# Performance work log

Hardware: AMD Instinct MI355X
Metric: run time of the kernel (lower is better)

Reference implementation:

```python
import jax, jax.numpy as jnp
import numpy as np

N_NODES = 100000


def gcn_conv(x, edge_index, W, b):
    """PyG-style GCNConv: linear transform, add self-loops, symmetric deg
    normalization, scatter-add aggregation, bias."""
    N = x.shape[0]
    h = x @ W  # [N, out]
    loops = jnp.arange(N, dtype=edge_index.dtype)
    src = jnp.concatenate([edge_index[0], loops])  # message sources (x_j)
    dst = jnp.concatenate([edge_index[1], loops])  # aggregation targets
    ones = jnp.ones(src.shape[0], dtype=h.dtype)
    deg = jax.ops.segment_sum(ones, dst, num_segments=N)
    dinv = jnp.where(deg > 0, jax.lax.rsqrt(deg), 0.0)
    norm = dinv[src] * dinv[dst]  # [E+N]
    msgs = h[src] * norm[:, None]  # gather + scale
    out = jax.ops.segment_sum(msgs, dst, num_segments=N)  # scatter-add
    return out + b


def setup_inputs() -> dict:
    key = jax.random.key(0)
    k1, k2, k3, k4, k5 = jax.random.split(key, 5)
    N, E, D, H = N_NODES, 3200000, 16, 16
    x = jax.random.normal(k1, (N, D), dtype=jnp.float32)
    edge_index = jax.random.randint(k2, (2, E), 0, N, dtype=jnp.int64)
    W1 = jax.random.normal(k3, (D, H), dtype=jnp.float32) / np.sqrt(D)
    b1 = jnp.zeros((H,), dtype=jnp.float32)
    W2 = jax.random.normal(k4, (H, 1), dtype=jnp.float32) / np.sqrt(H)
    b2 = jnp.zeros((1,), dtype=jnp.float32)
    return {"x": x, "edge_index": edge_index, "W1": W1, "b1": b1, "W2": W2, "b2": b2}


def reference(x, edge_index, W1, b1, W2, b2):
    h = jax.nn.relu(gcn_conv(x, edge_index, W1, b1))
    out = gcn_conv(h, edge_index, W2, b2)
    return jnp.squeeze(out, axis=-1)  # [N]
```

## Files before the change

kernel.cpp:

```cpp
#include <hip/hip_runtime.h>
#include <hip/hip_fp16.h>
#include <stdint.h>

#define TPB 256
#define TPBP 512
#define TPBR 512
#define NPB 256
#define LOG_NPB 8
#define MAXBINS 400
#define NCHUNK 512
#define CHUNK_CAP 6400
#define PCAP 48
#define PB2CAP 9216
#define START_MASK 0x1FFFFFFu

__global__ __launch_bounds__(TPBP) void k_place(const int* __restrict__ ei, int E,
                                                int chunkE, int nbins,
                                                int* __restrict__ baseT,
                                                uint32_t* __restrict__ part) {
    __shared__ uint32_t stage[CHUNK_CAP];
    __shared__ int sstart[MAXBINS];
    __shared__ int scnt[MAXBINS];
    __shared__ int scur[MAXBINS];
    int c = blockIdx.x, t = threadIdx.x;
    int es = c * chunkE, ee = min(E, es + chunkE), n = ee - es;
    for (int i = t; i < nbins; i += TPBP) scur[i] = 0;
    __syncthreads();
    const int* srcs = ei + es;
    const int* dsts = ei + E + es;
    int nv = n >> 2;
    bool al = ((((uintptr_t)srcs) | ((uintptr_t)dsts)) & 15) == 0;
    int4 sb[4], db[4];
    if (al) {
        const int4* s4 = (const int4*)srcs;
        const int4* d4 = (const int4*)dsts;
#pragma unroll
        for (int j = 0; j < 4; ++j) {
            int i = t + j * TPBP;
            if (i < nv) { sb[j] = s4[i]; db[j] = d4[i]; }
        }
#pragma unroll
        for (int j = 0; j < 4; ++j) {
            int i = t + j * TPBP;
            if (i < nv) {
                atomicAdd(&scur[db[j].x >> LOG_NPB], 1);
                atomicAdd(&scur[db[j].y >> LOG_NPB], 1);
                atomicAdd(&scur[db[j].z >> LOG_NPB], 1);
                atomicAdd(&scur[db[j].w >> LOG_NPB], 1);
            }
        }
        for (int i = 4 * nv + t; i < n; i += TPBP)
            atomicAdd(&scur[dsts[i] >> LOG_NPB], 1);
    } else {
        for (int i = t; i < n; i += TPBP)
            atomicAdd(&scur[dsts[i] >> LOG_NPB], 1);
    }
    __syncthreads();
    int val = (t < nbins) ? scur[t] : 0;
    __syncthreads();
    for (int off = 1; off < TPBP; off <<= 1) {
        int add = 0;
        if (t < nbins && t >= off) add = scur[t - off];
        __syncthreads();
        if (t < nbins) scur[t] += add;
        __syncthreads();
    }
    if (t < nbins) {
        sstart[t] = scur[t] - val;
        scnt[t] = val;
        baseT[(size_t)c * nbins + t] = val;
    }
    __syncthreads();
    if (t < nbins) scur[t] = sstart[t];
    __syncthreads();
    if (al) {
#pragma unroll
        for (int j = 0; j < 4; ++j) {
            int i = t + j * TPBP;
            if (i < nv) {
                int slot;
                slot = atomicAdd(&scur[db[j].x >> LOG_NPB], 1);
                stage[slot] = ((uint32_t)sb[j].x << LOG_NPB) | (uint32_t)(db[j].x & (NPB - 1));
                slot = atomicAdd(&scur[db[j].y >> LOG_NPB], 1);
                stage[slot] = ((uint32_t)sb[j].y << LOG_NPB) | (uint32_t)(db[j].y & (NPB - 1));
                slot = atomicAdd(&scur[db[j].z >> LOG_NPB], 1);
                stage[slot] = ((uint32_t)sb[j].z << LOG_NPB) | (uint32_t)(db[j].z & (NPB - 1));
                slot = atomicAdd(&scur[db[j].w >> LOG_NPB], 1);
                stage[slot] = ((uint32_t)sb[j].w << LOG_NPB) | (uint32_t)(db[j].w & (NPB - 1));
            }
        }
        for (int i = 4 * nv + t; i < n; i += TPBP) {
            int s = srcs[i], d = dsts[i];
            int slot = atomicAdd(&scur[d >> LOG_NPB], 1);
            stage[slot] = ((uint32_t)s << LOG_NPB) | (uint32_t)(d & (NPB - 1));
        }
    } else {
        for (int i = t; i < n; i += TPBP) {
            int s = srcs[i], d = dsts[i];
            int slot = atomicAdd(&scur[d >> LOG_NPB], 1);
            stage[slot] = ((uint32_t)s << LOG_NPB) | (uint32_t)(d & (NPB - 1));
        }
    }
    __syncthreads();
    int q = t >> 4, l = t & 15;
    for (int b = q; b < nbins; b += (TPBP >> 4)) {
        int l0 = sstart[b];
        int len = min(scnt[b], PCAP);
        size_t g0 = (size_t)b * ((size_t)NCHUNK * PCAP) + (size_t)c * PCAP;
        for (int i = l; i < len; i += 16)
            part[g0 + i] = stage[l0 + i];
    }
}

__global__ __launch_bounds__(TPBR) void k_rows(const uint32_t* __restrict__ part,
                                               const int* __restrict__ baseT,
                                               const float* __restrict__ x,
                                               const float* __restrict__ W1,
                                               uint32_t* __restrict__ rowInfo,
                                               float* __restrict__ dinv,
                                               int* __restrict__ part2,
                                               __half* __restrict__ g1h,
                                               int N, int nbins) {
    __shared__ int cnt[NPB];
    __shared__ int sbuf[NPB];
    __shared__ int cur[NPB];
    __shared__ int stage2[PB2CAP];
    __shared__ float Ws[256];
    int b = blockIdx.x, t = threadIdx.x;
    if (t < 256) Ws[t] = W1[t];
    if (t < NPB) cnt[t] = 0;
    __syncthreads();
    int my = min(baseT[(size_t)t * nbins + b], PCAP);
    const uint32_t* seg = part + (size_t)b * ((size_t)NCHUNK * PCAP) + (size_t)t * PCAP;
    for (int i = 0; i < my; ++i)
        atomicAdd(&cnt[seg[i] & (NPB - 1)], 1);
    __syncthreads();
    int deg = (t < NPB) ? cnt[t] : 0;
    if (t < NPB) sbuf[t] = deg;
    __syncthreads();
    for (int off = 1; off < NPB; off <<= 1) {
        int add = 0;
        if (t < NPB && t >= off) add = sbuf[t - off];
        __syncthreads();
        if (t < NPB) sbuf[t] += add;
        __syncthreads();
    }
    int excl = 0, total;
    if (t < NPB) {
        excl = sbuf[t] - deg;
        cur[t] = excl;
    }
    total = min(sbuf[NPB - 1], PB2CAP);
    int node = b * NPB + (t & (NPB - 1));
    float dv = rsqrtf(1.0f + (float)deg);
    if (t < NPB && node < N) {
        uint32_t dg = (uint32_t)min(deg, 127);
        rowInfo[node] = ((uint32_t)(b * PB2CAP + excl) & START_MASK) | (dg << 25);
        dinv[node] = dv;
    }
    __syncthreads();
    for (int i = 0; i < my; ++i) {
        uint32_t v = seg[i];
        int slot = atomicAdd(&cur[v & (NPB - 1)], 1);
        if (slot < PB2CAP) stage2[slot] = (int)(v >> LOG_NPB);
    }
    __syncthreads();
    int* p2 = part2 + (size_t)b * PB2CAP;
    for (int i = t; i < total; i += TPBR) p2[i] = stage2[i];
    if (t < NPB && node < N) {
        const float4* xv = (const float4*)(x + (size_t)node * 16);
        float4 a = xv[0], bb = xv[1], cc = xv[2], dd = xv[3];
        float xi[16] = {a.x, a.y, a.z, a.w, bb.x, bb.y, bb.z, bb.w,
                        cc.x, cc.y, cc.z, cc.w, dd.x, dd.y, dd.z, dd.w};
        __half2 hp[8];
#pragma unroll
        for (int j = 0; j < 8; ++j) {
            float o0 = 0.f, o1 = 0.f;
#pragma unroll
            for (int k = 0; k < 16; ++k) {
                o0 += xi[k] * Ws[k * 16 + 2 * j];
                o1 += xi[k] * Ws[k * 16 + 2 * j + 1];
            }
            hp[j] = __floats2half2_rn(o0 * dv, o1 * dv);
        }
        uint4* dst = (uint4*)(g1h + (size_t)node * 16);
        dst[0] = *(uint4*)&hp[0];
        dst[1] = *(uint4*)&hp[4];
    }
}

__global__ __launch_bounds__(256) void k_agg1_csr(const int* __restrict__ part2,
                                                  const uint32_t* __restrict__ rowInfo,
                                                  const __half* __restrict__ g1h,
                                                  const float* __restrict__ dinv,
                                                  const float* __restrict__ b1,
                                                  const float* __restrict__ W2,
                                                  float* __restrict__ g2, int N) {
    int wave = threadIdx.x >> 6, lane = threadIdx.x & 63;
    int n = blockIdx.x * 4 + wave;
    if (n >= N) return;
    int sub = lane >> 2;
    int j   = lane & 3;
    uint32_t info = rowInfo[n];
    int e0 = (int)(info & START_MASK);
    int e1 = e0 + (int)(info >> 25);
    float a0 = 0.f, a1 = 0.f, a2 = 0.f, a3 = 0.f;
    int e = e0 + sub;
    for (; e + 16 < e1; e += 32) {
        int s0 = part2[e];
        int s1 = part2[e + 16];
        uint2 u0 = *(const uint2*)(g1h + (size_t)s0 * 16 + 4 * j);
        uint2 u1 = *(const uint2*)(g1h + (size_t)s1 * 16 + 4 * j);
        float2 f;
        f = __half22float2(*(__half2*)&u0.x); a0 += f.x; a1 += f.y;
        f = __half22float2(*(__half2*)&u0.y); a2 += f.x; a3 += f.y;
        f = __half22float2(*(__half2*)&u1.x); a0 += f.x; a1 += f.y;
        f = __half22float2(*(__half2*)&u1.y); a2 += f.x; a3 += f.y;
    }
    for (; e < e1; e += 16) {
        int s0 = part2[e];
        uint2 u0 = *(const uint2*)(g1h + (size_t)s0 * 16 + 4 * j);
        float2 f;
        f = __half22float2(*(__half2*)&u0.x); a0 += f.x; a1 += f.y;
        f = __half22float2(*(__half2*)&u0.y); a2 += f.x; a3 += f.y;
    }
#pragma unroll
    for (int m = 4; m < 64; m <<= 1) {
        a0 += __shfl_xor(a0, m);
        a1 += __shfl_xor(a1, m);
        a2 += __shfl_xor(a2, m);
        a3 += __shfl_xor(a3, m);
    }
    {
        uint2 us = *(const uint2*)(g1h + (size_t)n * 16 + 4 * j);
        float2 f;
        f = __half22float2(*(__half2*)&us.x); a0 += f.x; a1 += f.y;
        f = __half22float2(*(__half2*)&us.y); a2 += f.x; a3 += f.y;
    }
    float di = dinv[n];
    float4 b1v = ((const float4*)b1)[j];
    float4 w2v = ((const float4*)W2)[j];
    float p = fmaxf(fmaf(a0, di, b1v.x), 0.f) * w2v.x
            + fmaxf(fmaf(a1, di, b1v.y), 0.f) * w2v.y
            + fmaxf(fmaf(a2, di, b1v.z), 0.f) * w2v.z
            + fmaxf(fmaf(a3, di, b1v.w), 0.f) * w2v.w;
    p += __shfl_xor(p, 1);
    p += __shfl_xor(p, 2);
    if (lane == 0) g2[n] = p * di;
}

__global__ __launch_bounds__(256) void k_agg2_csr(const int* __restrict__ part2,
                                                  const uint32_t* __restrict__ rowInfo,
                                                  const float* __restrict__ g2,
                                                  const float* __restrict__ dinv,
                                                  const float* __restrict__ b2,
                                                  float* __restrict__ out, int N) {
    int q = threadIdx.x >> 4, l = threadIdx.x & 15;
    int n = blockIdx.x * 16 + q;
    if (n >= N) return;
    uint32_t info = rowInfo[n];
    int e0 = (int)(info & START_MASK);
    int e1 = e0 + (int)(info >> 25);
    float acc = 0.f;
    for (int e = e0 + l; e < e1; e += 16)
        acc += g2[part2[e]];
    acc += __shfl_xor(acc, 1);
    acc += __shfl_xor(acc, 2);
    acc += __shfl_xor(acc, 4);
    acc += __shfl_xor(acc, 8);
    if (l == 0) out[n] = (acc + g2[n]) * dinv[n] + b2[0];
}

extern "C" void kernel_launch(void* const* d_in, const int* in_sizes, int n_in,
                              void* d_out, int out_size, void* d_ws, size_t ws_size,
                              hipStream_t stream) {
    const float* x  = (const float*)d_in[0];
    const int*   ei = (const int*)d_in[1];
    const float* W1 = (const float*)d_in[2];
    const float* b1 = (const float*)d_in[3];
    const float* W2 = (const float*)d_in[4];
    const float* b2 = (const float*)d_in[5];
    float* out = (float*)d_out;

    const int N = in_sizes[0] / 16;
    const int E = in_sizes[1] / 2;
    const int nbins = (N + NPB - 1) / NPB;
    const int chunkE = (((E + NCHUNK - 1) / NCHUNK) + 15) & ~15;

    float*    dinv    = (float*)d_ws;
    __half*   g1h     = (__half*)(dinv + N);
    uint32_t* part    = (uint32_t*)(g1h + (size_t)16 * N);
    int*      part2   = (int*)(part + (size_t)nbins * NCHUNK * PCAP);
    int*      baseT   = part2 + (size_t)nbins * PB2CAP;
    uint32_t* rowInfo = (uint32_t*)(baseT + (size_t)NCHUNK * nbins);
    float*    g2      = (float*)(rowInfo + N);

    k_place<<<NCHUNK, TPBP, 0, stream>>>(ei, E, chunkE, nbins, baseT, part);
    k_rows<<<nbins, TPBR, 0, stream>>>(part, baseT, x, W1, rowInfo, dinv, part2, g1h, N, nbins);
    k_agg1_csr<<<(N + 3) / 4, TPB, 0, stream>>>(part2, rowInfo, g1h, dinv, b1, W2, g2, N);
    k_agg2_csr<<<(N + 15) / 16, TPB, 0, stream>>>(part2, rowInfo, g2, dinv, b2, out, N);
}
```

Measured before the change: 170.1 us.

## Stage partition bins cooperatively in LDS and widen agg1 gathers to 16-byte loads

```diff
diff --git a/kernel.cpp b/kernel.cpp
--- a/kernel.cpp
+++ b/kernel.cpp
@@ -121,19 +121,47 @@
                                                int* __restrict__ part2,
                                                __half* __restrict__ g1h,
                                                int N, int nbins) {
+    __shared__ uint32_t stage2[PB2CAP];
+    __shared__ int scnt[NCHUNK];
+    __shared__ int soff[NCHUNK];
     __shared__ int cnt[NPB];
     __shared__ int sbuf[NPB];
     __shared__ int cur[NPB];
-    __shared__ int stage2[PB2CAP];
     __shared__ float Ws[256];
     int b = blockIdx.x, t = threadIdx.x;
     if (t < 256) Ws[t] = W1[t];
     if (t < NPB) cnt[t] = 0;
-    __syncthreads();
     int my = min(baseT[(size_t)t * nbins + b], PCAP);
-    const uint32_t* seg = part + (size_t)b * ((size_t)NCHUNK * PCAP) + (size_t)t * PCAP;
-    for (int i = 0; i < my; ++i)
-        atomicAdd(&cnt[seg[i] & (NPB - 1)], 1);
+    scnt[t] = my;
+    soff[t] = my;
+    __syncthreads();
+    for (int off = 1; off < TPBR; off <<= 1) {
+        int add = (t >= off) ? soff[t - off] : 0;
+        __syncthreads();
+        soff[t] += add;
+        __syncthreads();
+    }
+    int total = min(soff[TPBR - 1], PB2CAP);
+    int excl_s = soff[t] - my;
+    __syncthreads();
+    soff[t] = excl_s;
+    __syncthreads();
+    {
+        int g = t >> 4, l = t & 15;
+        const uint32_t* binBase = part + (size_t)b * ((size_t)NCHUNK * PCAP);
+        for (int s = g; s < NCHUNK; s += (TPBR >> 4)) {
+            int c2 = scnt[s];
+            int bs = soff[s];
+            const uint32_t* seg = binBase + (size_t)s * PCAP;
+            for (int i = l; i < c2; i += 16) {
+                int o = bs + i;
+                if (o < PB2CAP) stage2[o] = seg[i];
+            }
+        }
+    }
+    __syncthreads();
+    for (int i = t; i < total; i += TPBR)
+        atomicAdd(&cnt[stage2[i] & (NPB - 1)], 1);
     __syncthreads();
     int deg = (t < NPB) ? cnt[t] : 0;
     if (t < NPB) sbuf[t] = deg;
@@ -145,28 +173,24 @@
         if (t < NPB) sbuf[t] += add;
         __syncthreads();
     }
-    int excl = 0, total;
-    if (t < NPB) {
-        excl = sbuf[t] - deg;
-        cur[t] = excl;
-    }
-    total = min(sbuf[NPB - 1], PB2CAP);
     int node = b * NPB + (t & (NPB - 1));
     float dv = rsqrtf(1.0f + (float)deg);
-    if (t < NPB && node < N) {
-        uint32_t dg = (uint32_t)min(deg, 127);
-        rowInfo[node] = ((uint32_t)(b * PB2CAP + excl) & START_MASK) | (dg << 25);
-        dinv[node] = dv;
-    }
-    __syncthreads();
-    for (int i = 0; i < my; ++i) {
-        uint32_t v = seg[i];
+    if (t < NPB) {
+        int excl = sbuf[t] - deg;
+        cur[t] = excl;
+        if (node < N) {
+            uint32_t dg = (uint32_t)min(deg, 127);
+            rowInfo[node] = ((uint32_t)(b * PB2CAP + excl) & START_MASK) | (dg << 25);
+            dinv[node] = dv;
+        }
+    }
+    __syncthreads();
+    int* p2 = part2 + (size_t)b * PB2CAP;
+    for (int i = t; i < total; i += TPBR) {
+        uint32_t v = stage2[i];
         int slot = atomicAdd(&cur[v & (NPB - 1)], 1);
-        if (slot < PB2CAP) stage2[slot] = (int)(v >> LOG_NPB);
-    }
-    __syncthreads();
-    int* p2 = part2 + (size_t)b * PB2CAP;
-    for (int i = t; i < total; i += TPBR) p2[i] = stage2[i];
+        p2[slot] = (int)(v >> LOG_NPB);
+    }
     if (t < NPB && node < N) {
         const float4* xv = (const float4*)(x + (size_t)node * 16);
         float4 a = xv[0], bb = xv[1], cc = xv[2], dd = xv[3];
@@ -199,53 +223,57 @@
     int wave = threadIdx.x >> 6, lane = threadIdx.x & 63;
     int n = blockIdx.x * 4 + wave;
     if (n >= N) return;
-    int sub = lane >> 2;
-    int j   = lane & 3;
+    int j = lane & 1;
+    int sub = lane >> 1;
     uint32_t info = rowInfo[n];
     int e0 = (int)(info & START_MASK);
     int e1 = e0 + (int)(info >> 25);
     float a0 = 0.f, a1 = 0.f, a2 = 0.f, a3 = 0.f;
+    float a4 = 0.f, a5 = 0.f, a6 = 0.f, a7 = 0.f;
     int e = e0 + sub;
-    for (; e + 16 < e1; e += 32) {
+#define ACC8(U) { float2 f;                                            \
+        f = __half22float2(*(__half2*)&(U).x); a0 += f.x; a1 += f.y;   \
+        f = __half22float2(*(__half2*)&(U).y); a2 += f.x; a3 += f.y;   \
+        f = __half22float2(*(__half2*)&(U).z); a4 += f.x; a5 += f.y;   \
+        f = __half22float2(*(__half2*)&(U).w); a6 += f.x; a7 += f.y; }
+    for (; e + 32 < e1; e += 64) {
         int s0 = part2[e];
-        int s1 = part2[e + 16];
-        uint2 u0 = *(const uint2*)(g1h + (size_t)s0 * 16 + 4 * j);
-        uint2 u1 = *(const uint2*)(g1h + (size_t)s1 * 16 + 4 * j);
-        float2 f;
-        f = __half22float2(*(__half2*)&u0.x); a0 += f.x; a1 += f.y;
-        f = __half22float2(*(__half2*)&u0.y); a2 += f.x; a3 += f.y;
-        f = __half22float2(*(__half2*)&u1.x); a0 += f.x; a1 += f.y;
-        f = __half22float2(*(__half2*)&u1.y); a2 += f.x; a3 += f.y;
-    }
-    for (; e < e1; e += 16) {
+        int s1 = part2[e + 32];
+        uint4 u0 = *(const uint4*)(g1h + (size_t)s0 * 16 + 8 * j);
+        uint4 u1 = *(const uint4*)(g1h + (size_t)s1 * 16 + 8 * j);
+        ACC8(u0); ACC8(u1);
+    }
+    for (; e < e1; e += 32) {
         int s0 = part2[e];
-        uint2 u0 = *(const uint2*)(g1h + (size_t)s0 * 16 + 4 * j);
-        float2 f;
-        f = __half22float2(*(__half2*)&u0.x); a0 += f.x; a1 += f.y;
-        f = __half22float2(*(__half2*)&u0.y); a2 += f.x; a3 += f.y;
-    }
-#pragma unroll
-    for (int m = 4; m < 64; m <<= 1) {
-        a0 += __shfl_xor(a0, m);
-        a1 += __shfl_xor(a1, m);
-        a2 += __shfl_xor(a2, m);
-        a3 += __shfl_xor(a3, m);
+        uint4 u0 = *(const uint4*)(g1h + (size_t)s0 * 16 + 8 * j);
+        ACC8(u0);
+    }
+#pragma unroll
+    for (int m = 2; m < 64; m <<= 1) {
+        a0 += __shfl_xor(a0, m); a1 += __shfl_xor(a1, m);
+        a2 += __shfl_xor(a2, m); a3 += __shfl_xor(a3, m);
+        a4 += __shfl_xor(a4, m); a5 += __shfl_xor(a5, m);
+        a6 += __shfl_xor(a6, m); a7 += __shfl_xor(a7, m);
     }
     {
-        uint2 us = *(const uint2*)(g1h + (size_t)n * 16 + 4 * j);
-        float2 f;
-        f = __half22float2(*(__half2*)&us.x); a0 += f.x; a1 += f.y;
-        f = __half22float2(*(__half2*)&us.y); a2 += f.x; a3 += f.y;
-    }
+        uint4 us = *(const uint4*)(g1h + (size_t)n * 16 + 8 * j);
+        ACC8(us);
+    }
+#undef ACC8
     float di = dinv[n];
-    float4 b1v = ((const float4*)b1)[j];
-    float4 w2v = ((const float4*)W2)[j];
-    float p = fmaxf(fmaf(a0, di, b1v.x), 0.f) * w2v.x
-            + fmaxf(fmaf(a1, di, b1v.y), 0.f) * w2v.y
-            + fmaxf(fmaf(a2, di, b1v.z), 0.f) * w2v.z
-            + fmaxf(fmaf(a3, di, b1v.w), 0.f) * w2v.w;
+    float4 b1a = ((const float4*)b1)[2 * j];
+    float4 b1b = ((const float4*)b1)[2 * j + 1];
+    float4 w2a = ((const float4*)W2)[2 * j];
+    float4 w2b = ((const float4*)W2)[2 * j + 1];
+    float p = fmaxf(fmaf(a0, di, b1a.x), 0.f) * w2a.x
+            + fmaxf(fmaf(a1, di, b1a.y), 0.f) * w2a.y
+            + fmaxf(fmaf(a2, di, b1a.z), 0.f) * w2a.z
+            + fmaxf(fmaf(a3, di, b1a.w), 0.f) * w2a.w
+            + fmaxf(fmaf(a4, di, b1b.x), 0.f) * w2b.x
+            + fmaxf(fmaf(a5, di, b1b.y), 0.f) * w2b.y
+            + fmaxf(fmaf(a6, di, b1b.z), 0.f) * w2b.z
+            + fmaxf(fmaf(a7, di, b1b.w), 0.f) * w2b.w;
     p += __shfl_xor(p, 1);
-    p += __shfl_xor(p, 2);
     if (lane == 0) g2[n] = p * di;
 }
 
```

Measured after the change: 183.6 us. 1.08x slower.

## Stage bin edges cooperatively in shared memory and shrink agg1 groups to 16 lanes

Applied to the files above, without the earlier changes.

```diff
diff --git a/kernel.cpp b/kernel.cpp
--- a/kernel.cpp
+++ b/kernel.cpp
@@ -121,19 +121,47 @@
                                                int* __restrict__ part2,
                                                __half* __restrict__ g1h,
                                                int N, int nbins) {
+    __shared__ uint32_t stage2[PB2CAP];
+    __shared__ int scnt[NCHUNK];
+    __shared__ int soff[NCHUNK];
     __shared__ int cnt[NPB];
     __shared__ int sbuf[NPB];
     __shared__ int cur[NPB];
-    __shared__ int stage2[PB2CAP];
     __shared__ float Ws[256];
     int b = blockIdx.x, t = threadIdx.x;
     if (t < 256) Ws[t] = W1[t];
     if (t < NPB) cnt[t] = 0;
-    __syncthreads();
     int my = min(baseT[(size_t)t * nbins + b], PCAP);
-    const uint32_t* seg = part + (size_t)b * ((size_t)NCHUNK * PCAP) + (size_t)t * PCAP;
-    for (int i = 0; i < my; ++i)
-        atomicAdd(&cnt[seg[i] & (NPB - 1)], 1);
+    scnt[t] = my;
+    soff[t] = my;
+    __syncthreads();
+    for (int off = 1; off < TPBR; off <<= 1) {
+        int add = (t >= off) ? soff[t - off] : 0;
+        __syncthreads();
+        soff[t] += add;
+        __syncthreads();
+    }
+    int total = min(soff[TPBR - 1], PB2CAP);
+    int excl_s = soff[t] - my;
+    __syncthreads();
+    soff[t] = excl_s;
+    __syncthreads();
+    {
+        int g = t >> 4, l = t & 15;
+        const uint32_t* binBase = part + (size_t)b * ((size_t)NCHUNK * PCAP);
+        for (int s = g; s < NCHUNK; s += (TPBR >> 4)) {
+            int c2 = scnt[s];
+            int bs = soff[s];
+            const uint32_t* seg = binBase + (size_t)s * PCAP;
+            for (int i = l; i < c2; i += 16) {
+                int o = bs + i;
+                if (o < PB2CAP) stage2[o] = seg[i];
+            }
+        }
+    }
+    __syncthreads();
+    for (int i = t; i < total; i += TPBR)
+        atomicAdd(&cnt[stage2[i] & (NPB - 1)], 1);
     __syncthreads();
     int deg = (t < NPB) ? cnt[t] : 0;
     if (t < NPB) sbuf[t] = deg;
@@ -145,28 +173,24 @@
         if (t < NPB) sbuf[t] += add;
         __syncthreads();
     }
-    int excl = 0, total;
-    if (t < NPB) {
-        excl = sbuf[t] - deg;
-        cur[t] = excl;
-    }
-    total = min(sbuf[NPB - 1], PB2CAP);
     int node = b * NPB + (t & (NPB - 1));
     float dv = rsqrtf(1.0f + (float)deg);
-    if (t < NPB && node < N) {
-        uint32_t dg = (uint32_t)min(deg, 127);
-        rowInfo[node] = ((uint32_t)(b * PB2CAP + excl) & START_MASK) | (dg << 25);
-        dinv[node] = dv;
-    }
-    __syncthreads();
-    for (int i = 0; i < my; ++i) {
-        uint32_t v = seg[i];
+    if (t < NPB) {
+        int excl = sbuf[t] - deg;
+        cur[t] = excl;
+        if (node < N) {
+            uint32_t dg = (uint32_t)min(deg, 127);
+            rowInfo[node] = ((uint32_t)(b * PB2CAP + excl) & START_MASK) | (dg << 25);
+            dinv[node] = dv;
+        }
+    }
+    __syncthreads();
+    int* p2 = part2 + (size_t)b * PB2CAP;
+    for (int i = t; i < total; i += TPBR) {
+        uint32_t v = stage2[i];
         int slot = atomicAdd(&cur[v & (NPB - 1)], 1);
-        if (slot < PB2CAP) stage2[slot] = (int)(v >> LOG_NPB);
-    }
-    __syncthreads();
-    int* p2 = part2 + (size_t)b * PB2CAP;
-    for (int i = t; i < total; i += TPBR) p2[i] = stage2[i];
+        p2[slot] = (int)(v >> LOG_NPB);
+    }
     if (t < NPB && node < N) {
         const float4* xv = (const float4*)(x + (size_t)node * 16);
         float4 a = xv[0], bb = xv[1], cc = xv[2], dd = xv[3];
@@ -196,19 +220,20 @@
                                                   const float* __restrict__ b1,
                                                   const float* __restrict__ W2,
                                                   float* __restrict__ g2, int N) {
-    int wave = threadIdx.x >> 6, lane = threadIdx.x & 63;
-    int n = blockIdx.x * 4 + wave;
+    int g = threadIdx.x >> 4;
+    int l = threadIdx.x & 15;
+    int sub = l >> 2;
+    int j   = l & 3;
+    int n = blockIdx.x * 16 + g;
     if (n >= N) return;
-    int sub = lane >> 2;
-    int j   = lane & 3;
     uint32_t info = rowInfo[n];
     int e0 = (int)(info & START_MASK);
     int e1 = e0 + (int)(info >> 25);
     float a0 = 0.f, a1 = 0.f, a2 = 0.f, a3 = 0.f;
     int e = e0 + sub;
-    for (; e + 16 < e1; e += 32) {
+    for (; e + 4 < e1; e += 8) {
         int s0 = part2[e];
-        int s1 = part2[e + 16];
+        int s1 = part2[e + 4];
         uint2 u0 = *(const uint2*)(g1h + (size_t)s0 * 16 + 4 * j);
         uint2 u1 = *(const uint2*)(g1h + (size_t)s1 * 16 + 4 * j);
         float2 f;
@@ -217,20 +242,17 @@
         f = __half22float2(*(__half2*)&u1.x); a0 += f.x; a1 += f.y;
         f = __half22float2(*(__half2*)&u1.y); a2 += f.x; a3 += f.y;
     }
-    for (; e < e1; e += 16) {
+    for (; e < e1; e += 4) {
         int s0 = part2[e];
         uint2 u0 = *(const uint2*)(g1h + (size_t)s0 * 16 + 4 * j);
         float2 f;
         f = __half22float2(*(__half2*)&u0.x); a0 += f.x; a1 += f.y;
         f = __half22float2(*(__half2*)&u0.y); a2 += f.x; a3 += f.y;
     }
-#pragma unroll
-    for (int m = 4; m < 64; m <<= 1) {
-        a0 += __shfl_xor(a0, m);
-        a1 += __shfl_xor(a1, m);
-        a2 += __shfl_xor(a2, m);
-        a3 += __shfl_xor(a3, m);
-    }
+    a0 += __shfl_xor(a0, 4); a1 += __shfl_xor(a1, 4);
+    a2 += __shfl_xor(a2, 4); a3 += __shfl_xor(a3, 4);
+    a0 += __shfl_xor(a0, 8); a1 += __shfl_xor(a1, 8);
+    a2 += __shfl_xor(a2, 8); a3 += __shfl_xor(a3, 8);
     {
         uint2 us = *(const uint2*)(g1h + (size_t)n * 16 + 4 * j);
         float2 f;
@@ -246,7 +268,7 @@
             + fmaxf(fmaf(a3, di, b1v.w), 0.f) * w2v.w;
     p += __shfl_xor(p, 1);
     p += __shfl_xor(p, 2);
-    if (lane == 0) g2[n] = p * di;
+    if (l == 0) g2[n] = p * di;
 }
 
 __global__ __launch_bounds__(256) void k_agg2_csr(const int* __restrict__ part2,
@@ -297,6 +319,6 @@
 
     k_place<<<NCHUNK, TPBP, 0, stream>>>(ei, E, chunkE, nbins, baseT, part);
     k_rows<<<nbins, TPBR, 0, stream>>>(part, baseT, x, W1, rowInfo, dinv, part2, g1h, N, nbins);
-    k_agg1_csr<<<(N + 3) / 4, TPB, 0, stream>>>(part2, rowInfo, g1h, dinv, b1, W2, g2, N);
+    k_agg1_csr<<<(N + 15) / 16, TPB, 0, stream>>>(part2, rowInfo, g1h, dinv, b1, W2, g2, N);
     k_agg2_csr<<<(N + 15) / 16, TPB, 0, stream>>>(part2, rowInfo, g2, dinv, b2, out, N);
 }
```

Measured after the change: 164.0 us. -3.6%, faster.
